# Performance work log

Hardware: AMD Instinct MI355X
Metric: run time of the kernel (lower is better)

## Reference

```python
import jax, jax.numpy as jnp
import numpy as np

SCALES = (8, 16, 32)
RATIOS = (0.5, 1.0, 2.0)
STRIDE = 16
K = len(SCALES) * len(RATIOS)
PRE_NMS = 6000
POST_NMS = 2000
NMS_THRESH = 0.7
ROIS_PER_IMG = 128
FG_ROIS = 32
FG_THRESH = 0.5
BG_HI = 0.5
BG_LO = 0.1
NUM_GT = 20
BBOX_CLIP = 4.135  # log(1000/16), standard delta clamp


def _generate_anchors(image_width, image_height):
    base = float(STRIDE)
    ctr = (base - 1.0) / 2.0
    size = base * base
    ratios = np.array(RATIOS, dtype=np.float64)
    scales = np.array(SCALES, dtype=np.float64)
    ws = np.round(np.sqrt(size / ratios))
    hs = np.round(ws * ratios)
    ws = (ws[:, None] * scales[None, :]).reshape(-1)  # (K,) ratio-major
    hs = (hs[:, None] * scales[None, :]).reshape(-1)
    anchors = np.stack([ctr - 0.5 * (ws - 1), ctr - 0.5 * (hs - 1),
                        ctr + 0.5 * (ws - 1), ctr + 0.5 * (hs - 1)], axis=1)  # (K,4)
    fw = image_width // STRIDE
    fh = image_height // STRIDE
    sx = np.arange(fw) * STRIDE
    sy = np.arange(fh) * STRIDE
    sxx, syy = np.meshgrid(sx, sy)  # (fh, fw)
    shifts = np.stack([sxx.ravel(), syy.ravel(), sxx.ravel(), syy.ravel()], axis=1)  # (fh*fw,4)
    all_anchors = (shifts[:, None, :] + anchors[None, :, :]).reshape(-1, 4)  # (fh*fw*K,4), K fastest
    return jnp.asarray(all_anchors, jnp.float32)


def _conv2d(x, w, b):
    y = jax.lax.conv_general_dilated(x, w, (1, 1), 'SAME',
                                     dimension_numbers=('NHWC', 'HWIO', 'NHWC'))
    return y + b


def _bbox_transform_inv(anchors, deltas):
    w = anchors[:, 2] - anchors[:, 0] + 1.0
    h = anchors[:, 3] - anchors[:, 1] + 1.0
    cx = anchors[:, 0] + 0.5 * w
    cy = anchors[:, 1] + 0.5 * h
    dx, dy = deltas[:, 0], deltas[:, 1]
    dw = jnp.clip(deltas[:, 2], -BBOX_CLIP, BBOX_CLIP)
    dh = jnp.clip(deltas[:, 3], -BBOX_CLIP, BBOX_CLIP)
    pcx = dx * w + cx
    pcy = dy * h + cy
    pw = jnp.exp(dw) * w
    ph = jnp.exp(dh) * h
    return jnp.stack([pcx - 0.5 * pw, pcy - 0.5 * ph,
                      pcx + 0.5 * pw, pcy + 0.5 * ph], axis=1)


def _pairwise_iou(a, b):
    area_a = (a[:, 2] - a[:, 0] + 1.0) * (a[:, 3] - a[:, 1] + 1.0)
    area_b = (b[:, 2] - b[:, 0] + 1.0) * (b[:, 3] - b[:, 1] + 1.0)
    xx1 = jnp.maximum(a[:, None, 0], b[None, :, 0])
    yy1 = jnp.maximum(a[:, None, 1], b[None, :, 1])
    xx2 = jnp.minimum(a[:, None, 2], b[None, :, 2])
    yy2 = jnp.minimum(a[:, None, 3], b[None, :, 3])
    iw = jnp.clip(xx2 - xx1 + 1.0, 0.0)
    ih = jnp.clip(yy2 - yy1 + 1.0, 0.0)
    inter = iw * ih
    return inter / (area_a[:, None] + area_b[None, :] - inter)


def _nms_keep(boxes, thresh):
    # boxes assumed sorted by score descending; greedy suppression
    n = boxes.shape[0]
    iou = _pairwise_iou(boxes, boxes)  # (n, n)
    idx = jnp.arange(n)
    def body(i, keep):
        sup = (iou[i] > thresh) & (idx > i)
        return jnp.where(keep[i], keep & ~sup, keep)
    return jax.lax.fori_loop(0, n, body, jnp.ones((n,), jnp.bool_))


def _forward(inputs, w_shared, b_shared, w_cls, b_cls, w_bbox, b_bbox,
             gt_boxes, image_width, image_height):
    fh = image_height // STRIDE
    fw = image_width // STRIDE
    anchors = _generate_anchors(image_width, image_height)  # (fh*fw*K, 4)

    shared = _conv2d(inputs, w_shared, b_shared)
    rpn_cls_score = _conv2d(shared, w_cls, b_cls)      # (1, fh, fw, 2K)
    rpn_bbox_pred = _conv2d(shared, w_bbox, b_bbox)    # (1, fh, fw, 4K)

    # softmax over the 2 (bg, fg) channels per anchor
    cls_prob = jax.nn.softmax(rpn_cls_score.reshape(1, fh, fw, K, 2), axis=-1)
    fg_scores = cls_prob[..., 1].reshape(-1)           # (fh*fw*K,)
    deltas = rpn_bbox_pred.reshape(-1, 4)              # (fh*fw*K, 4)

    # ---- proposal_layer ----
    proposals = _bbox_transform_inv(anchors, deltas)
    proposals = jnp.stack([
        jnp.clip(proposals[:, 0], 0.0, image_width - 1.0),
        jnp.clip(proposals[:, 1], 0.0, image_height - 1.0),
        jnp.clip(proposals[:, 2], 0.0, image_width - 1.0),
        jnp.clip(proposals[:, 3], 0.0, image_height - 1.0)], axis=1)

    top_scores, order = jax.lax.top_k(fg_scores, PRE_NMS)
    top_boxes = proposals[order]                       # (PRE_NMS, 4), score-sorted

    keep = _nms_keep(jax.lax.stop_gradient(top_boxes), NMS_THRESH)
    n = PRE_NMS
    rank = jnp.where(keep, jnp.arange(n), n + jnp.arange(n))
    sel = jnp.argsort(rank)[:POST_NMS]                 # kept boxes first, score order
    roi_boxes = top_boxes[sel]                         # (POST_NMS, 4)
    roi_scores = top_scores[sel]
    rois = jnp.concatenate([jnp.zeros((POST_NMS, 1), roi_boxes.dtype), roi_boxes], axis=1)

    # ---- proposal_target_layer (deterministic top-k sampling) ----
    ov = _pairwise_iou(roi_boxes, gt_boxes[:, :4])     # (POST_NMS, NUM_GT)
    max_ov = ov.max(axis=1)
    fg_key = jnp.where(max_ov >= FG_THRESH, max_ov, -1.0)
    _, fg_idx = jax.lax.top_k(fg_key, FG_ROIS)
    bg_key = jnp.where((max_ov < BG_HI) & (max_ov >= BG_LO), max_ov, -1.0)
    _, bg_idx = jax.lax.top_k(bg_key, ROIS_PER_IMG - FG_ROIS)
    keep_inds = jnp.concatenate([fg_idx, bg_idx])      # (128,)
    return rois[keep_inds]                             # (128, 5)


def setup_inputs() -> dict:
    key = jax.random.key(0)
    ks = jax.random.split(key, 10)
    C_in, C_mid = 1024, 256
    inputs = jax.random.normal(ks[0], (1, 64, 64, C_in), jnp.float32)
    w_shared = jax.random.normal(ks[1], (3, 3, C_in, C_mid), jnp.float32) * np.sqrt(2.0 / (9 * C_in))
    b_shared = jnp.zeros((C_mid,), jnp.float32)
    w_cls = jax.random.normal(ks[2], (1, 1, C_mid, 2 * K), jnp.float32) * np.sqrt(2.0 / C_mid)
    b_cls = jnp.zeros((2 * K,), jnp.float32)
    w_bbox = jax.random.normal(ks[3], (1, 1, C_mid, 4 * K), jnp.float32) * (0.1 * np.sqrt(2.0 / C_mid))
    b_bbox = jnp.zeros((4 * K,), jnp.float32)
    # valid gt boxes inside a 1024x1024 image
    cx = jax.random.uniform(ks[4], (NUM_GT,), minval=100.0, maxval=900.0)
    cy = jax.random.uniform(ks[5], (NUM_GT,), minval=100.0, maxval=900.0)
    bw = jax.random.uniform(ks[6], (NUM_GT,), minval=32.0, maxval=300.0)
    bh = jax.random.uniform(ks[7], (NUM_GT,), minval=32.0, maxval=300.0)
    cls = jax.random.randint(ks[8], (NUM_GT,), 1, 21).astype(jnp.float32)
    gt_boxes = jnp.stack([jnp.clip(cx - bw / 2, 0.0, 1023.0), jnp.clip(cy - bh / 2, 0.0, 1023.0),
                          jnp.clip(cx + bw / 2, 0.0, 1023.0), jnp.clip(cy + bh / 2, 0.0, 1023.0),
                          cls], axis=1)
    return {"inputs": inputs, "w_shared": w_shared, "b_shared": b_shared,
            "w_cls": w_cls, "b_cls": b_cls, "w_bbox": w_bbox, "b_bbox": b_bbox,
            "gt_boxes": gt_boxes, "image_width": 1024, "image_height": 1024}


def reference(inputs, w_shared, b_shared, w_cls, b_cls, w_bbox, b_bbox,
              gt_boxes, image_width, image_height):
    return _forward(inputs, w_shared, b_shared, w_cls, b_cls, w_bbox, b_bbox,
                    gt_boxes, image_width, image_height)
```

## Files before the change

### kernel.cpp

```cpp
#include <hip/hip_runtime.h>
#include <cstdint>
#include <cstddef>

#define M_POS 4096
#define NCH   256
#define KTOT  9216
#define NANCH 36864
#define NSORT 65536
#define PRE   6000
#define POST  2000
#define NGRP  94
#define MROW  6016
#define NSLOT 14

typedef unsigned long long u64;
typedef unsigned int u32;

__device__ __forceinline__ u32 ord_f32(float f) {
  u32 u = __float_as_uint(f);
  return (u & 0x80000000u) ? ~u : (u | 0x80000000u);
}

__global__ __launch_bounds__(256) void conv3x3(const float* __restrict__ in,
                                               const float* __restrict__ wgt,
                                               float* __restrict__ part,
                                               int kPer) {
  __shared__ __align__(16) float As[16][128];
  __shared__ __align__(16) float Bs[16][64];
  int tid = threadIdx.x;
  int bm = blockIdx.x << 7;
  int bn = blockIdx.y << 6;
  int kBeg = blockIdx.z * kPer;
  int am = tid & 127;
  int aq = (tid >> 7) << 2;
  int gm = bm + am;
  int y = gm >> 6, x = gm & 63;
  int bkk = tid >> 4;
  int bn4 = (tid & 15) << 2;
  int ty = tid >> 4, tx = tid & 15;

  float acc[8][4];
#pragma unroll
  for (int i = 0; i < 8; ++i)
#pragma unroll
    for (int j = 0; j < 4; ++j) acc[i][j] = 0.f;

  for (int k0 = kBeg; k0 < kBeg + kPer; k0 += 16) {
#pragma unroll
    for (int p = 0; p < 2; ++p) {
      int kk = aq + (p << 3);
      int k = k0 + kk;
      int tap = k >> 10;
      int c = k & 1023;
      int iy = y + tap / 3 - 1;
      int ix = x + tap % 3 - 1;
      float4 v = make_float4(0.f, 0.f, 0.f, 0.f);
      if (iy >= 0 && iy < 64 && ix >= 0 && ix < 64)
        v = *(const float4*)(in + (size_t)((((iy << 6) + ix) << 10) + c));
      As[kk + 0][am] = v.x;
      As[kk + 1][am] = v.y;
      As[kk + 2][am] = v.z;
      As[kk + 3][am] = v.w;
    }
    *(float4*)&Bs[bkk][bn4] =
        *(const float4*)(wgt + (size_t)(k0 + bkk) * NCH + bn + bn4);
    __syncthreads();
#pragma unroll
    for (int kk = 0; kk < 16; ++kk) {
      float4 a0 = *(const float4*)&As[kk][ty << 2];
      float4 a1 = *(const float4*)&As[kk][64 + (ty << 2)];
      float4 b0 = *(const float4*)&Bs[kk][tx << 2];
      float a[8] = {a0.x, a0.y, a0.z, a0.w, a1.x, a1.y, a1.z, a1.w};
      float b[4] = {b0.x, b0.y, b0.z, b0.w};
#pragma unroll
      for (int i = 0; i < 8; ++i)
#pragma unroll
        for (int j = 0; j < 4; ++j) acc[i][j] += a[i] * b[j];
    }
    __syncthreads();
  }
  size_t ob = (size_t)blockIdx.z * ((size_t)M_POS * NCH);
#pragma unroll
  for (int i = 0; i < 8; ++i) {
    int row = bm + ((i < 4) ? ((ty << 2) + i) : (64 + (ty << 2) + i - 4));
    float4 o = make_float4(acc[i][0], acc[i][1], acc[i][2], acc[i][3]);
    *(float4*)(part + ob + (size_t)row * NCH + bn + (tx << 2)) = o;
  }
}

__global__ __launch_bounds__(256) void reduce_bias(const float* __restrict__ part,
                                                   const float* __restrict__ bias,
                                                   float* __restrict__ outp, int ks) {
  int idx = blockIdx.x * 256 + threadIdx.x;
  float v = 0.f;
  for (int s = 0; s < ks; ++s) v += part[(size_t)s * (M_POS * NCH) + idx];
  outp[idx] = v + bias[idx & 255];
}

__global__ __launch_bounds__(64) void conv1x1(const float* __restrict__ sh,
                                              const float* __restrict__ wc,
                                              const float* __restrict__ bc,
                                              const float* __restrict__ wb,
                                              const float* __restrict__ bb2,
                                              float* __restrict__ cls,
                                              float* __restrict__ bbox) {
  __shared__ float row[256];
  int pos = blockIdx.x;
  int tid = threadIdx.x;
  *(float4*)&row[tid * 4] = *(const float4*)(sh + (size_t)pos * 256 + tid * 4);
  __syncthreads();
  if (tid < 18) {
    float acc = bc[tid];
    for (int c = 0; c < 256; ++c) acc += row[c] * wc[c * 18 + tid];
    cls[(size_t)pos * 18 + tid] = acc;
  } else if (tid < 54) {
    int n = tid - 18;
    float acc = bb2[n];
    for (int c = 0; c < 256; ++c) acc += row[c] * wb[c * 36 + n];
    bbox[(size_t)pos * 36 + n] = acc;
  }
}

__global__ __launch_bounds__(256) void proposals_k(const float* __restrict__ cls,
                                                   const float* __restrict__ bb,
                                                   u64* __restrict__ keys,
                                                   float* __restrict__ prop) {
  int idx = blockIdx.x * 256 + threadIdx.x;
  if (idx >= NANCH) return;
  int a = idx % 9;
  int pos = idx / 9;
  int x = pos & 63, y = pos >> 6;
  float s0 = cls[(size_t)pos * 18 + 2 * a];
  float s1 = cls[(size_t)pos * 18 + 2 * a + 1];
  float mx = fmaxf(s0, s1);
  float e0 = expf(s0 - mx), e1 = expf(s1 - mx);
  float score = e1 / (e0 + e1);
  u32 u = ord_f32(score);
  keys[idx] = ((u64)u << 32) | (u64)(0xFFFFFFFFu - (u32)idx);
  const float AW[9] = {184.f, 368.f, 736.f, 128.f, 256.f, 512.f, 88.f, 176.f, 352.f};
  const float AH[9] = {96.f, 192.f, 384.f, 128.f, 256.f, 512.f, 176.f, 352.f, 704.f};
  float w = AW[a], h = AH[a];
  float cx = (float)(x * 16) + 8.0f;
  float cy = (float)(y * 16) + 8.0f;
  float dx = bb[(size_t)pos * 36 + 4 * a + 0];
  float dy = bb[(size_t)pos * 36 + 4 * a + 1];
  float dw = bb[(size_t)pos * 36 + 4 * a + 2];
  float dh = bb[(size_t)pos * 36 + 4 * a + 3];
  dw = fminf(fmaxf(dw, -4.135f), 4.135f);
  dh = fminf(fmaxf(dh, -4.135f), 4.135f);
  float pcx = dx * w + cx;
  float pcy = dy * h + cy;
  float pw = expf(dw) * w;
  float ph = expf(dh) * h;
  float x1 = pcx - 0.5f * pw, y1 = pcy - 0.5f * ph;
  float x2 = pcx + 0.5f * pw, y2 = pcy + 0.5f * ph;
  x1 = fminf(fmaxf(x1, 0.f), 1023.f);
  y1 = fminf(fmaxf(y1, 0.f), 1023.f);
  x2 = fminf(fmaxf(x2, 0.f), 1023.f);
  y2 = fminf(fmaxf(y2, 0.f), 1023.f);
  prop[(size_t)idx * 4 + 0] = x1;
  prop[(size_t)idx * 4 + 1] = y1;
  prop[(size_t)idx * 4 + 2] = x2;
  prop[(size_t)idx * 4 + 3] = y2;
}

__global__ __launch_bounds__(1024) void sort_local(u64* keys) {
  __shared__ u64 s[2048];
  int base = blockIdx.x * 2048;
  s[threadIdx.x] = keys[base + threadIdx.x];
  s[threadIdx.x + 1024] = keys[base + threadIdx.x + 1024];
  __syncthreads();
  for (int k = 2; k <= 2048; k <<= 1) {
    for (int j = k >> 1; j >= 1; j >>= 1) {
      int t = threadIdx.x;
      int i = ((t & ~(j - 1)) << 1) | (t & (j - 1));
      int p = i | j;
      bool desc = (((base + i) & k) == 0);
      u64 a = s[i], b = s[p];
      if (desc ? (a < b) : (a > b)) { s[i] = b; s[p] = a; }
      __syncthreads();
    }
  }
  keys[base + threadIdx.x] = s[threadIdx.x];
  keys[base + threadIdx.x + 1024] = s[threadIdx.x + 1024];
}

__device__ __forceinline__ void cmpswap(u64& a, u64& b, bool desc) {
  if (desc ? (a < b) : (a > b)) { u64 t = a; a = b; b = t; }
}

template <int L>
__global__ __launch_bounds__(256) void gstep_n(u64* keys, int k, int j) {
  const int jl = j >> (L - 1);
  int t = blockIdx.x * 256 + threadIdx.x;
  int base = ((t & ~(jl - 1)) << L) | (t & (jl - 1));
  bool desc = ((base & k) == 0);
  u64 v[1 << L];
#pragma unroll
  for (int m = 0; m < (1 << L); ++m) v[m] = keys[base + m * jl];
#pragma unroll
  for (int l = 0; l < L; ++l) {
    int s = 1 << (L - 1 - l);
#pragma unroll
    for (int m = 0; m < (1 << L); ++m)
      if ((m & s) == 0) cmpswap(v[m], v[m | s], desc);
  }
#pragma unroll
  for (int m = 0; m < (1 << L); ++m) keys[base + m * jl] = v[m];
}

__global__ __launch_bounds__(1024) void sort_lstep(u64* keys, int k) {
  __shared__ u64 s[2048];
  int base = blockIdx.x * 2048;
  s[threadIdx.x] = keys[base + threadIdx.x];
  s[threadIdx.x + 1024] = keys[base + threadIdx.x + 1024];
  __syncthreads();
  for (int j = 1024; j >= 1; j >>= 1) {
    int t = threadIdx.x;
    int i = ((t & ~(j - 1)) << 1) | (t & (j - 1));
    int p = i | j;
    bool desc = (((base + i) & k) == 0);
    u64 a = s[i], b = s[p];
    if (desc ? (a < b) : (a > b)) { s[i] = b; s[p] = a; }
    __syncthreads();
  }
  keys[base + threadIdx.x] = s[threadIdx.x];
  keys[base + threadIdx.x + 1024] = s[threadIdx.x + 1024];
}

__global__ __launch_bounds__(256) void gather_top(const u64* __restrict__ keys,
                                                  const float4* __restrict__ prop,
                                                  float4* __restrict__ topbox) {
  int i = blockIdx.x * 256 + threadIdx.x;
  if (i >= PRE) return;
  u64 kk = keys[i];
  u32 idx = 0xFFFFFFFFu - (u32)(kk & 0xFFFFFFFFull);
  topbox[i] = prop[idx];
}

__global__ __launch_bounds__(64) void nms_mask(const float4* __restrict__ boxes,
                                               u64* __restrict__ maskT) {
  int ci = blockIdx.x, ri = blockIdx.y;
  if (ci < ri) return;
  __shared__ float4 cb[64];
  int t = threadIdx.x;
  int col = (ci << 6) + t;
  cb[t] = (col < PRE) ? boxes[col] : make_float4(0.f, 0.f, 0.f, 0.f);
  __syncthreads();
  int r = (ri << 6) + t;
  if (r >= PRE) return;
  float4 rb = boxes[r];
  float ra = (rb.z - rb.x + 1.f) * (rb.w - rb.y + 1.f);
  u64 bits = 0ull;
  for (int cc = 0; cc < 64; ++cc) {
    int j = (ci << 6) + cc;
    if (j > r && j < PRE) {
      float4 b = cb[cc];
      float ba = (b.z - b.x + 1.f) * (b.w - b.y + 1.f);
      float xx1 = fmaxf(rb.x, b.x), yy1 = fmaxf(rb.y, b.y);
      float xx2 = fminf(rb.z, b.z), yy2 = fminf(rb.w, b.w);
      float iw = fmaxf(xx2 - xx1 + 1.f, 0.f);
      float ih = fmaxf(yy2 - yy1 + 1.f, 0.f);
      float inter = iw * ih;
      float iou = inter / (ra + ba - inter);
      if (iou > 0.7f) bits |= (1ull << cc);
    }
  }
  maskT[(size_t)ci * MROW + r] = bits;
}

__global__ __launch_bounds__(512) void nms_tail(const u64* __restrict__ maskT,
                                                const float4* __restrict__ topbox,
                                                const float* __restrict__ gt,
                                                float* __restrict__ out) {
  __shared__ u64 keepL[NGRP];
  __shared__ u64 keepS;
  __shared__ u64 extS;
  __shared__ u32 exitS;
  __shared__ float4 roibL[POST];
  __shared__ float mov[POST];
  __shared__ u64 sk[2048];
  __shared__ float gtb[20][4];
  __shared__ int fgsel[32];
  __shared__ int bgsel[96];
  __shared__ u32 wscan[NGRP + 1];

  const int tid = threadIdx.x;
  const int lane = tid & 63, wv = tid >> 6;

  u64 acc[NSLOT], v[NSLOT];
#pragma unroll
  for (int i = 0; i < NSLOT; ++i) { acc[i] = 0ull; v[i] = 0ull; }
  if (wv > 0) {
#pragma unroll
    for (int i = 0; i < NSLOT; ++i) {
      int gp = wv + 7 * i;
      if (gp < NGRP) v[i] = maskT[(size_t)gp * MROW + lane];
    }
  }
  u64 x = 0ull;
  if (wv == 0) x = maskT[lane];
  u32 keptTot = 0;

  for (int g = 0; g < NGRP; ++g) {
    if (wv == 0) {
      u64 cur = 0ull;
      if (g > 0) {
        u64 e = extS;
        u32 elo = __builtin_amdgcn_readfirstlane((u32)(e & 0xFFFFFFFFull));
        u32 ehi = __builtin_amdgcn_readfirstlane((u32)(e >> 32));
        cur = ((u64)ehi << 32) | (u64)elo;
      }
      u32 xlo = (u32)(x & 0xFFFFFFFFull);
      u32 xhi = (u32)(x >> 32);
      u64 keep = 0ull;
#pragma unroll
      for (int t = 0; t < 64; ++t) {
        u32 mlo = __builtin_amdgcn_readlane(xlo, t);
        u32 mhi = __builtin_amdgcn_readlane(xhi, t);
        u64 mt = ((u64)mhi << 32) | (u64)mlo;
        u64 sup = (cur >> t) & 1ull;
        u64 sel = sup - 1ull;
        keep |= (1ull << t) & sel;
        cur |= mt & sel;
      }
      if (g == NGRP - 1) keep &= (1ull << 48) - 1ull;
      keptTot += (u32)__popcll(keep);
      if (lane == 0) {
        keepS = keep;
        exitS = (keptTot >= POST) ? 1u : 0u;
        keepL[g] = keep;
      }
      if (g + 1 < NGRP) {
        int ii = ((g + 1) << 6) + lane;
        x = (ii < PRE) ? maskT[(size_t)(g + 1) * MROW + ii] : 0ull;
      }
    }
    asm volatile("s_waitcnt lgkmcnt(0)" ::: "memory");
    __builtin_amdgcn_sched_barrier(0);
    __builtin_amdgcn_s_barrier();
    __builtin_amdgcn_sched_barrier(0);
    u32 ex = exitS;
    u64 kb = keepS;
    if (ex) {
      for (int z = g + 1 + tid; z < NGRP; z += 512) keepL[z] = 0ull;
      break;
    }
    if (wv > 0) {
      u64 sel2 = ((kb >> lane) & 1ull) ? ~0ull : 0ull;
      u64 e = 0ull;
      bool own = false;
#pragma unroll
      for (int i = 0; i < NSLOT; ++i) {
        int gp = wv + 7 * i;
        if (gp < NGRP && gp > g) {
          acc[i] |= (v[i] & sel2);
          if (gp == g + 1) { e = acc[i]; own = true; }
        }
      }
      if (own) {
#pragma unroll
        for (int s = 1; s < 64; s <<= 1) e |= __shfl_xor(e, s, 64);
        if (lane == 0) extS = e;
      }
      int col = ((g + 1) << 6) + lane;
#pragma unroll
      for (int i = 0; i < NSLOT; ++i) {
        int gp = wv + 7 * i;
        if (gp < NGRP && gp > g + 1) v[i] = maskT[(size_t)gp * MROW + col];
      }
    }
    asm volatile("s_waitcnt lgkmcnt(0)" ::: "memory");
    __builtin_amdgcn_sched_barrier(0);
    __builtin_amdgcn_s_barrier();
    __builtin_amdgcn_sched_barrier(0);
  }

  __syncthreads();
  if (tid == 0) {
    u32 r = 0;
    for (int g2 = 0; g2 < NGRP; ++g2) {
      wscan[g2] = r;
      r += (u32)__popcll(keepL[g2]);
    }
    wscan[NGRP] = r;
  }
  __syncthreads();
  u32 ktot = wscan[NGRP];
  for (int i = tid; i < PRE; i += 512) {
    int g2 = i >> 6, t2 = i & 63;
    u64 wk = keepL[g2];
    bool kept = (wk >> t2) & 1ull;
    u32 pk = wscan[g2] + (u32)__popcll(wk & ((1ull << t2) - 1ull));
    u32 pos = kept ? pk : (ktot + (u32)i - pk);
    if (pos < POST) roibL[pos] = topbox[i];
  }
  __syncthreads();

  if (tid < 20) {
    gtb[tid][0] = gt[tid * 5 + 0];
    gtb[tid][1] = gt[tid * 5 + 1];
    gtb[tid][2] = gt[tid * 5 + 2];
    gtb[tid][3] = gt[tid * 5 + 3];
  }
  __syncthreads();
  for (int i = tid; i < POST; i += 512) {
    float4 b = roibL[i];
    float aa = (b.z - b.x + 1.f) * (b.w - b.y + 1.f);
    float m = -3.402823466e38f;
    for (int t = 0; t < 20; ++t) {
      float gx1 = gtb[t][0], gy1 = gtb[t][1], gx2 = gtb[t][2], gy2 = gtb[t][3];
      float ga = (gx2 - gx1 + 1.f) * (gy2 - gy1 + 1.f);
      float xx1 = fmaxf(b.x, gx1), yy1 = fmaxf(b.y, gy1);
      float xx2 = fminf(b.z, gx2), yy2 = fminf(b.w, gy2);
      float iw = fmaxf(xx2 - xx1 + 1.f, 0.f);
      float ih = fmaxf(yy2 - yy1 + 1.f, 0.f);
      float inter = iw * ih;
      float iou = inter / (aa + ga - inter);
      m = fmaxf(m, iou);
    }
    mov[i] = m;
  }
  __syncthreads();
  for (int i = tid; i < 2048; i += 512) {
    float key;
    if (i < POST) { float vv = mov[i]; key = (vv >= 0.5f) ? vv : -1.0f; }
    else key = -2.0f;
    sk[i] = ((u64)ord_f32(key) << 32) | (u64)(2047u - (u32)i);
  }
  __syncthreads();
  for (int k = 2; k <= 2048; k <<= 1) {
    for (int j = k >> 1; j >= 1; j >>= 1) {
#pragma unroll
      for (int q = 0; q < 2; ++q) {
        int t = tid + (q << 9);
        int i = ((t & ~(j - 1)) << 1) | (t & (j - 1));
        int p = i | j;
        bool desc = ((i & k) == 0);
        u64 a = sk[i], b = sk[p];
        if (desc ? (a < b) : (a > b)) { sk[i] = b; sk[p] = a; }
      }
      __syncthreads();
    }
  }
  if (tid < 32) fgsel[tid] = (int)(2047u - (u32)(sk[tid] & 0xFFFFFFFFull));
  __syncthreads();
  for (int i = tid; i < 2048; i += 512) {
    float key;
    if (i < POST) {
      float vv = mov[i];
      key = (vv < 0.5f && vv >= 0.1f) ? vv : -1.0f;
    } else key = -2.0f;
    sk[i] = ((u64)ord_f32(key) << 32) | (u64)(2047u - (u32)i);
  }
  __syncthreads();
  for (int k = 2; k <= 2048; k <<= 1) {
    for (int j = k >> 1; j >= 1; j >>= 1) {
#pragma unroll
      for (int q = 0; q < 2; ++q) {
        int t = tid + (q << 9);
        int i = ((t & ~(j - 1)) << 1) | (t & (j - 1));
        int p = i | j;
        bool desc = ((i & k) == 0);
        u64 a = sk[i], b = sk[p];
        if (desc ? (a < b) : (a > b)) { sk[i] = b; sk[p] = a; }
      }
      __syncthreads();
    }
  }
  if (tid < 96) bgsel[tid] = (int)(2047u - (u32)(sk[tid] & 0xFFFFFFFFull));
  __syncthreads();
  if (tid < 128) {
    int idx = (tid < 32) ? fgsel[tid] : bgsel[tid - 32];
    float4 b = roibL[idx];
    out[tid * 5 + 0] = 0.f;
    out[tid * 5 + 1] = b.x;
    out[tid * 5 + 2] = b.y;
    out[tid * 5 + 3] = b.z;
    out[tid * 5 + 4] = b.w;
  }
}

extern "C" void kernel_launch(void* const* d_in, const int* in_sizes, int n_in,
                              void* d_out, int out_size, void* d_ws, size_t ws_size,
                              hipStream_t stream) {
  const float* in   = (const float*)d_in[0];
  const float* wsh  = (const float*)d_in[1];
  const float* bsh  = (const float*)d_in[2];
  const float* wcls = (const float*)d_in[3];
  const float* bcls = (const float*)d_in[4];
  const float* wbb  = (const float*)d_in[5];
  const float* bbb  = (const float*)d_in[6];
  const float* gt   = (const float*)d_in[7];

  char* w = (char*)d_ws;
  const size_t OFF_SHARED = 0;
  const size_t OFF_CLS    = 4194304;
  const size_t OFF_BBOX   = 4489216;
  const size_t OFF_PROP   = 5226496;
  const size_t OFF_KEYS   = 0;
  const size_t OFF_TOPBOX = 524288;
  const size_t OFF_MASK   = 620288;
  const size_t OFF_PART   = 5816320;

  float* sharedb = (float*)(w + OFF_SHARED);
  float* cls     = (float*)(w + OFF_CLS);
  float* bbox    = (float*)(w + OFF_BBOX);
  float* prop    = (float*)(w + OFF_PROP);
  u64*   keys    = (u64*)(w + OFF_KEYS);
  float4* topbox = (float4*)(w + OFF_TOPBOX);
  u64*   maskT   = (u64*)(w + OFF_MASK);
  float* out     = (float*)d_out;

  const size_t SLICE = (size_t)M_POS * NCH * 4;
  int KS = 1;
  if      (ws_size >= OFF_PART + 16 * SLICE) KS = 16;
  else if (ws_size >= OFF_PART + 8 * SLICE)  KS = 8;
  else if (ws_size >= OFF_PART + 4 * SLICE)  KS = 4;
  else if (ws_size >= OFF_PART + 2 * SLICE)  KS = 2;
  float* part = (KS > 1) ? (float*)(w + OFF_PART) : sharedb;

  conv3x3<<<dim3(32, 4, KS), 256, 0, stream>>>(in, wsh, part, KTOT / KS);
  reduce_bias<<<4096, 256, 0, stream>>>(part, bsh, sharedb, KS);
  conv1x1<<<4096, 64, 0, stream>>>(sharedb, wcls, bcls, wbb, bbb, cls, bbox);
  hipMemsetAsync(w + (size_t)NANCH * 8, 0, (size_t)(NSORT - NANCH) * 8, stream);
  proposals_k<<<144, 256, 0, stream>>>(cls, bbox, keys, prop);
  sort_local<<<32, 1024, 0, stream>>>(keys);
  gstep_n<1><<<128, 256, 0, stream>>>(keys, 4096, 2048);
  sort_lstep<<<32, 1024, 0, stream>>>(keys, 4096);
  gstep_n<2><<<64, 256, 0, stream>>>(keys, 8192, 4096);
  sort_lstep<<<32, 1024, 0, stream>>>(keys, 8192);
  gstep_n<3><<<32, 256, 0, stream>>>(keys, 16384, 8192);
  sort_lstep<<<32, 1024, 0, stream>>>(keys, 16384);
  gstep_n<4><<<16, 256, 0, stream>>>(keys, 32768, 16384);
  sort_lstep<<<32, 1024, 0, stream>>>(keys, 32768);
  gstep_n<5><<<8, 256, 0, stream>>>(keys, 65536, 32768);
  sort_lstep<<<32, 1024, 0, stream>>>(keys, 65536);

  gather_top<<<24, 256, 0, stream>>>(keys, (const float4*)prop, topbox);
  nms_mask<<<dim3(NGRP, NGRP), 64, 0, stream>>>(topbox, maskT);
  nms_tail<<<1, 512, 0, stream>>>(maskT, topbox, gt, out);
}
```

Before: 593.7 us.

## Retune conv split, batch conv1x1, split NMS tail, rebalance sort global steps

Reduces the conv3x3 split-K factor ceiling from 16 to 8 to cut partial-sum traffic in the reduction. conv1x1 now processes four positions per 256-thread block, and the memset of the sort padding is folded into proposals_k. The last two bitonic global merge steps are split into more, smaller launches so more blocks run in parallel. The single-block NMS tail is split into a scan kernel and a 1024-thread selection kernel, which adds a launch and a global round trip for the keep words.

```diff
diff --git a/kernel.cpp b/kernel.cpp
--- a/kernel.cpp
+++ b/kernel.cpp
@@ -97,26 +97,28 @@
   outp[idx] = v + bias[idx & 255];
 }
 
-__global__ __launch_bounds__(64) void conv1x1(const float* __restrict__ sh,
-                                              const float* __restrict__ wc,
-                                              const float* __restrict__ bc,
-                                              const float* __restrict__ wb,
-                                              const float* __restrict__ bb2,
-                                              float* __restrict__ cls,
-                                              float* __restrict__ bbox) {
-  __shared__ float row[256];
-  int pos = blockIdx.x;
+__global__ __launch_bounds__(256) void conv1x1(const float* __restrict__ sh,
+                                               const float* __restrict__ wc,
+                                               const float* __restrict__ bc,
+                                               const float* __restrict__ wb,
+                                               const float* __restrict__ bb2,
+                                               float* __restrict__ cls,
+                                               float* __restrict__ bbox) {
+  __shared__ float row[4][260];
   int tid = threadIdx.x;
-  *(float4*)&row[tid * 4] = *(const float4*)(sh + (size_t)pos * 256 + tid * 4);
-  __syncthreads();
-  if (tid < 18) {
-    float acc = bc[tid];
-    for (int c = 0; c < 256; ++c) acc += row[c] * wc[c * 18 + tid];
-    cls[(size_t)pos * 18 + tid] = acc;
-  } else if (tid < 54) {
-    int n = tid - 18;
+  int g = tid >> 6, lane = tid & 63;
+  int pos = (blockIdx.x << 2) + g;
+  *(float4*)&row[g][lane * 4] =
+      *(const float4*)(sh + (size_t)pos * 256 + lane * 4);
+  __syncthreads();
+  if (lane < 18) {
+    float acc = bc[lane];
+    for (int c = 0; c < 256; ++c) acc += row[g][c] * wc[c * 18 + lane];
+    cls[(size_t)pos * 18 + lane] = acc;
+  } else if (lane < 54) {
+    int n = lane - 18;
     float acc = bb2[n];
-    for (int c = 0; c < 256; ++c) acc += row[c] * wb[c * 36 + n];
+    for (int c = 0; c < 256; ++c) acc += row[g][c] * wb[c * 36 + n];
     bbox[(size_t)pos * 36 + n] = acc;
   }
 }
@@ -126,7 +128,8 @@
                                                    u64* __restrict__ keys,
                                                    float* __restrict__ prop) {
   int idx = blockIdx.x * 256 + threadIdx.x;
-  if (idx >= NANCH) return;
+  if (idx >= NSORT) return;
+  if (idx >= NANCH) { keys[idx] = 0ull; return; }
   int a = idx % 9;
   int pos = idx / 9;
   int x = pos & 63, y = pos >> 6;
@@ -269,28 +272,18 @@
   maskT[(size_t)ci * MROW + r] = bits;
 }
 
-__global__ __launch_bounds__(512) void nms_tail(const u64* __restrict__ maskT,
-                                                const float4* __restrict__ topbox,
-                                                const float* __restrict__ gt,
-                                                float* __restrict__ out) {
-  __shared__ u64 keepL[NGRP];
+__global__ __launch_bounds__(512, 2) void nms_scan(const u64* __restrict__ maskT,
+                                                   u64* __restrict__ keepw) {
   __shared__ u64 keepS;
   __shared__ u64 extS;
   __shared__ u32 exitS;
-  __shared__ float4 roibL[POST];
-  __shared__ float mov[POST];
-  __shared__ u64 sk[2048];
-  __shared__ float gtb[20][4];
-  __shared__ int fgsel[32];
-  __shared__ int bgsel[96];
-  __shared__ u32 wscan[NGRP + 1];
-
   const int tid = threadIdx.x;
   const int lane = tid & 63, wv = tid >> 6;
 
   u64 acc[NSLOT], v[NSLOT];
 #pragma unroll
   for (int i = 0; i < NSLOT; ++i) { acc[i] = 0ull; v[i] = 0ull; }
+
   if (wv > 0) {
 #pragma unroll
     for (int i = 0; i < NSLOT; ++i) {
@@ -329,7 +322,7 @@
       if (lane == 0) {
         keepS = keep;
         exitS = (keptTot >= POST) ? 1u : 0u;
-        keepL[g] = keep;
+        keepw[g] = keep;
       }
       if (g + 1 < NGRP) {
         int ii = ((g + 1) << 6) + lane;
@@ -343,8 +336,8 @@
     u32 ex = exitS;
     u64 kb = keepS;
     if (ex) {
-      for (int z = g + 1 + tid; z < NGRP; z += 512) keepL[z] = 0ull;
-      break;
+      for (int z = g + 1 + tid; z < NGRP; z += 512) keepw[z] = 0ull;
+      return;
     }
     if (wv > 0) {
       u64 sel2 = ((kb >> lane) & 1ull) ? ~0ull : 0ull;
@@ -375,28 +368,39 @@
     __builtin_amdgcn_s_barrier();
     __builtin_amdgcn_sched_barrier(0);
   }
-
-  __syncthreads();
+}
+
+__global__ __launch_bounds__(1024) void tail2(const u64* __restrict__ keepw,
+                                              const float4* __restrict__ topbox,
+                                              const float* __restrict__ gt,
+                                              float* __restrict__ out) {
+  __shared__ float4 roibL[POST];
+  __shared__ float mov[POST];
+  __shared__ u64 sk[2048];
+  __shared__ u32 wscan[NGRP + 1];
+  __shared__ float gtb[20][4];
+  __shared__ int fgsel[32];
+  __shared__ int bgsel[96];
+  int tid = threadIdx.x;
+
   if (tid == 0) {
     u32 r = 0;
-    for (int g2 = 0; g2 < NGRP; ++g2) {
-      wscan[g2] = r;
-      r += (u32)__popcll(keepL[g2]);
+    for (int g = 0; g < NGRP; ++g) {
+      wscan[g] = r;
+      r += (u32)__popcll(keepw[g]);
     }
     wscan[NGRP] = r;
   }
   __syncthreads();
   u32 ktot = wscan[NGRP];
-  for (int i = tid; i < PRE; i += 512) {
-    int g2 = i >> 6, t2 = i & 63;
-    u64 wk = keepL[g2];
-    bool kept = (wk >> t2) & 1ull;
-    u32 pk = wscan[g2] + (u32)__popcll(wk & ((1ull << t2) - 1ull));
+  for (int i = tid; i < PRE; i += 1024) {
+    int g = i >> 6, t = i & 63;
+    u64 wk = keepw[g];
+    bool kept = (wk >> t) & 1ull;
+    u32 pk = wscan[g] + (u32)__popcll(wk & ((1ull << t) - 1ull));
     u32 pos = kept ? pk : (ktot + (u32)i - pk);
     if (pos < POST) roibL[pos] = topbox[i];
   }
-  __syncthreads();
-
   if (tid < 20) {
     gtb[tid][0] = gt[tid * 5 + 0];
     gtb[tid][1] = gt[tid * 5 + 1];
@@ -404,7 +408,7 @@
     gtb[tid][3] = gt[tid * 5 + 3];
   }
   __syncthreads();
-  for (int i = tid; i < POST; i += 512) {
+  for (int i = tid; i < POST; i += 1024) {
     float4 b = roibL[i];
     float aa = (b.z - b.x + 1.f) * (b.w - b.y + 1.f);
     float m = -3.402823466e38f;
@@ -422,7 +426,7 @@
     mov[i] = m;
   }
   __syncthreads();
-  for (int i = tid; i < 2048; i += 512) {
+  for (int i = tid; i < 2048; i += 1024) {
     float key;
     if (i < POST) { float vv = mov[i]; key = (vv >= 0.5f) ? vv : -1.0f; }
     else key = -2.0f;
@@ -431,21 +435,18 @@
   __syncthreads();
   for (int k = 2; k <= 2048; k <<= 1) {
     for (int j = k >> 1; j >= 1; j >>= 1) {
-#pragma unroll
-      for (int q = 0; q < 2; ++q) {
-        int t = tid + (q << 9);
-        int i = ((t & ~(j - 1)) << 1) | (t & (j - 1));
-        int p = i | j;
-        bool desc = ((i & k) == 0);
-        u64 a = sk[i], b = sk[p];
-        if (desc ? (a < b) : (a > b)) { sk[i] = b; sk[p] = a; }
-      }
+      int t = tid;
+      int i = ((t & ~(j - 1)) << 1) | (t & (j - 1));
+      int p = i | j;
+      bool desc = ((i & k) == 0);
+      u64 a = sk[i], b = sk[p];
+      if (desc ? (a < b) : (a > b)) { sk[i] = b; sk[p] = a; }
       __syncthreads();
     }
   }
   if (tid < 32) fgsel[tid] = (int)(2047u - (u32)(sk[tid] & 0xFFFFFFFFull));
   __syncthreads();
-  for (int i = tid; i < 2048; i += 512) {
+  for (int i = tid; i < 2048; i += 1024) {
     float key;
     if (i < POST) {
       float vv = mov[i];
@@ -456,15 +457,12 @@
   __syncthreads();
   for (int k = 2; k <= 2048; k <<= 1) {
     for (int j = k >> 1; j >= 1; j >>= 1) {
-#pragma unroll
-      for (int q = 0; q < 2; ++q) {
-        int t = tid + (q << 9);
-        int i = ((t & ~(j - 1)) << 1) | (t & (j - 1));
-        int p = i | j;
-        bool desc = ((i & k) == 0);
-        u64 a = sk[i], b = sk[p];
-        if (desc ? (a < b) : (a > b)) { sk[i] = b; sk[p] = a; }
-      }
+      int t = tid;
+      int i = ((t & ~(j - 1)) << 1) | (t & (j - 1));
+      int p = i | j;
+      bool desc = ((i & k) == 0);
+      u64 a = sk[i], b = sk[p];
+      if (desc ? (a < b) : (a > b)) { sk[i] = b; sk[p] = a; }
       __syncthreads();
     }
   }
@@ -501,6 +499,7 @@
   const size_t OFF_KEYS   = 0;
   const size_t OFF_TOPBOX = 524288;
   const size_t OFF_MASK   = 620288;
+  const size_t OFF_KEEPW  = 5144320;
   const size_t OFF_PART   = 5816320;
 
   float* sharedb = (float*)(w + OFF_SHARED);
@@ -510,21 +509,20 @@
   u64*   keys    = (u64*)(w + OFF_KEYS);
   float4* topbox = (float4*)(w + OFF_TOPBOX);
   u64*   maskT   = (u64*)(w + OFF_MASK);
+  u64*   keepw   = (u64*)(w + OFF_KEEPW);
   float* out     = (float*)d_out;
 
   const size_t SLICE = (size_t)M_POS * NCH * 4;
   int KS = 1;
-  if      (ws_size >= OFF_PART + 16 * SLICE) KS = 16;
-  else if (ws_size >= OFF_PART + 8 * SLICE)  KS = 8;
-  else if (ws_size >= OFF_PART + 4 * SLICE)  KS = 4;
-  else if (ws_size >= OFF_PART + 2 * SLICE)  KS = 2;
+  if      (ws_size >= OFF_PART + 8 * SLICE) KS = 8;
+  else if (ws_size >= OFF_PART + 4 * SLICE) KS = 4;
+  else if (ws_size >= OFF_PART + 2 * SLICE) KS = 2;
   float* part = (KS > 1) ? (float*)(w + OFF_PART) : sharedb;
 
   conv3x3<<<dim3(32, 4, KS), 256, 0, stream>>>(in, wsh, part, KTOT / KS);
   reduce_bias<<<4096, 256, 0, stream>>>(part, bsh, sharedb, KS);
-  conv1x1<<<4096, 64, 0, stream>>>(sharedb, wcls, bcls, wbb, bbb, cls, bbox);
-  hipMemsetAsync(w + (size_t)NANCH * 8, 0, (size_t)(NSORT - NANCH) * 8, stream);
-  proposals_k<<<144, 256, 0, stream>>>(cls, bbox, keys, prop);
+  conv1x1<<<1024, 256, 0, stream>>>(sharedb, wcls, bcls, wbb, bbb, cls, bbox);
+  proposals_k<<<256, 256, 0, stream>>>(cls, bbox, keys, prop);
   sort_local<<<32, 1024, 0, stream>>>(keys);
   gstep_n<1><<<128, 256, 0, stream>>>(keys, 4096, 2048);
   sort_lstep<<<32, 1024, 0, stream>>>(keys, 4096);
@@ -532,12 +530,15 @@
   sort_lstep<<<32, 1024, 0, stream>>>(keys, 8192);
   gstep_n<3><<<32, 256, 0, stream>>>(keys, 16384, 8192);
   sort_lstep<<<32, 1024, 0, stream>>>(keys, 16384);
-  gstep_n<4><<<16, 256, 0, stream>>>(keys, 32768, 16384);
+  gstep_n<3><<<32, 256, 0, stream>>>(keys, 32768, 16384);
+  gstep_n<1><<<128, 256, 0, stream>>>(keys, 32768, 2048);
   sort_lstep<<<32, 1024, 0, stream>>>(keys, 32768);
-  gstep_n<5><<<8, 256, 0, stream>>>(keys, 65536, 32768);
+  gstep_n<3><<<32, 256, 0, stream>>>(keys, 65536, 32768);
+  gstep_n<2><<<64, 256, 0, stream>>>(keys, 65536, 4096);
   sort_lstep<<<32, 1024, 0, stream>>>(keys, 65536);
 
   gather_top<<<24, 256, 0, stream>>>(keys, (const float4*)prop, topbox);
   nms_mask<<<dim3(NGRP, NGRP), 64, 0, stream>>>(topbox, maskT);
-  nms_tail<<<1, 512, 0, stream>>>(maskT, topbox, gt, out);
-}
+  nms_scan<<<1, 512, 0, stream>>>(maskT, keepw);
+  tail2<<<1, 1024, 0, stream>>>(keepw, topbox, gt, out);
+}
```

Result: no change. 591.4 us (-0.4%).
